# Performance work log

Hardware: AMD Instinct MI355X
Metric: run time of the kernel (lower is better)

The kernel has to match this reference:

```python
import jax, jax.numpy as jnp
import numpy as np

D_MODEL = 768; N_LAYER = 4; D_STATE = 64; D_CONV = 4; EXPAND = 2; HEADDIM = 64
D_INNER = EXPAND * D_MODEL          # 1536
NHEADS = D_INNER // HEADDIM         # 24
CONV_DIM = D_INNER + 2 * D_STATE    # 1664
D_IN_PROJ = 2 * D_INNER + 2 * D_STATE + NHEADS  # 3224
VOCAB = 50257; EPS = 1e-5


def _ln(x, w, b):
    m = x.mean(-1, keepdims=True)
    v = ((x - m) ** 2).mean(-1, keepdims=True)
    return (x - m) * jax.lax.rsqrt(v + EPS) * w + b


def _silu(x):
    return x * jax.nn.sigmoid(x)


def _mamba2(x, W_in, conv_w, conv_b, dt_bias, A_log, Dp, rms_w, W_out):
    # x: [B, L, d_model]
    Bsz, L, _ = x.shape
    zxbcdt = x @ W_in.T                                   # [B,L,D_IN_PROJ]
    z = zxbcdt[..., :D_INNER]
    xBC = zxbcdt[..., D_INNER:D_INNER + CONV_DIM]
    dt = zxbcdt[..., D_INNER + CONV_DIM:]                 # [B,L,H]
    # causal depthwise conv over time
    xc = jnp.transpose(xBC, (0, 2, 1))                    # [B,C,L]
    xc = jax.lax.conv_general_dilated(
        xc, conv_w[:, None, :], (1,), [(D_CONV - 1, 0)],
        dimension_numbers=('NCH', 'OIH', 'NCH'), feature_group_count=CONV_DIM)
    xBC = _silu(jnp.transpose(xc, (0, 2, 1)) + conv_b)
    xh = xBC[..., :D_INNER].reshape(Bsz, L, NHEADS, HEADDIM)
    Bc = xBC[..., D_INNER:D_INNER + D_STATE]              # [B,L,N]
    Cc = xBC[..., D_INNER + D_STATE:]                     # [B,L,N]
    dt = jax.nn.softplus(dt + dt_bias)                    # [B,L,H]
    dA = jnp.exp(dt * (-jnp.exp(A_log)))                  # [B,L,H]

    def step(h, inp):
        dA_t, dt_t, x_t, B_t, C_t = inp
        h = dA_t[:, :, None, None] * h + (dt_t[:, :, None] * x_t)[..., None] * B_t[:, None, None, :]
        return h, jnp.einsum('bhpn,bn->bhp', h, C_t)

    tm = lambda a: jnp.moveaxis(a, 1, 0)  # time-major
    h0 = jnp.zeros((Bsz, NHEADS, HEADDIM, D_STATE), x.dtype)
    _, y = jax.lax.scan(step, h0, (tm(dA), tm(dt), tm(xh), tm(Bc), tm(Cc)))
    y = jnp.moveaxis(y, 0, 1) + Dp[:, None] * xh          # [B,L,H,P]
    y = y.reshape(Bsz, L, D_INNER) * _silu(z)             # gate
    y = y * jax.lax.rsqrt((y * y).mean(-1, keepdims=True) + EPS) * rms_w
    return y @ W_out.T


def setup_inputs() -> dict:
    key = jax.random.key(0)
    ks = jax.random.split(key, 16)
    B, L = 1, 1024
    idx = jax.random.randint(ks[0], (B, L), 0, VOCAB)
    targets = jax.random.randint(ks[1], (B, L), 0, VOCAB)
    s = 0.02
    emb = jax.random.normal(ks[2], (VOCAB, D_MODEL), jnp.float32) * s
    ln_w = jnp.ones((N_LAYER, D_MODEL)); ln_b = jnp.zeros((N_LAYER, D_MODEL))
    W_in = jax.random.normal(ks[3], (N_LAYER, D_IN_PROJ, D_MODEL), jnp.float32) * s
    conv_w = jax.random.normal(ks[4], (N_LAYER, CONV_DIM, D_CONV), jnp.float32) * 0.1
    conv_b = jnp.zeros((N_LAYER, CONV_DIM))
    dt_bias = jnp.log(jnp.expm1(jax.random.uniform(ks[5], (N_LAYER, NHEADS), minval=0.001, maxval=0.1)))
    A_log = jnp.log(jax.random.uniform(ks[6], (N_LAYER, NHEADS), minval=1.0, maxval=16.0))
    Dp = jnp.ones((N_LAYER, NHEADS))
    rms_w = jnp.ones((N_LAYER, D_INNER))
    W_out = jax.random.normal(ks[7], (N_LAYER, D_MODEL, D_INNER), jnp.float32) * s
    lnf_w = jnp.ones((D_MODEL,)); lnf_b = jnp.zeros((D_MODEL,))
    return {"idx": idx, "targets": targets, "emb": emb, "ln_w": ln_w, "ln_b": ln_b,
            "W_in": W_in, "conv_w": conv_w, "conv_b": conv_b, "dt_bias": dt_bias,
            "A_log": A_log, "Dp": Dp, "rms_w": rms_w, "W_out": W_out,
            "lnf_w": lnf_w, "lnf_b": lnf_b}


def reference(idx, targets, emb, ln_w, ln_b, W_in, conv_w, conv_b, dt_bias,
              A_log, Dp, rms_w, W_out, lnf_w, lnf_b):
    x = emb[idx]                                          # [B,L,D]
    for i in range(N_LAYER):
        x = x + _mamba2(_ln(x, ln_w[i], ln_b[i]), W_in[i], conv_w[i], conv_b[i],
                        dt_bias[i], A_log[i], Dp[i], rms_w[i], W_out[i])
    x = _ln(x, lnf_w, lnf_b)
    logits = x @ emb.T                                    # tied head
    logp = jax.nn.log_softmax(logits, axis=-1)
    loss = -jnp.take_along_axis(logp, targets[..., None], axis=-1).mean()
    return logits, loss
```

## Files before the change

kernel.cpp:

```cpp
#include <hip/hip_runtime.h>
#include <hip/hip_bf16.h>
#include <math.h>

#define SL     1024
#define DMODEL 768
#define NLAYER 4
#define NSTATE 64
#define HEADDIM 64
#define DINNER 1536
#define NHEADS 24
#define CONVDIM 1664
#define DINPROJ 3224
#define VOCABN 50257

typedef __attribute__((ext_vector_type(8))) short short8;
typedef __attribute__((ext_vector_type(4))) short short4v;
typedef __attribute__((ext_vector_type(4))) float f32x4;

__device__ __forceinline__ short f2bf(float f) {
    unsigned int u = __builtin_bit_cast(unsigned int, f);
    u += 0x7fffu + ((u >> 16) & 1u);
    return (short)(u >> 16);
}

#define AS1 __attribute__((address_space(1)))
#define AS3 __attribute__((address_space(3)))
__device__ __forceinline__ void gl2lds16(const void* g, void* l) {
    __builtin_amdgcn_global_load_lds((const AS1 unsigned int*)g,
                                     (AS3 unsigned int*)(unsigned int)(uintptr_t)l,
                                     16, 0, 0);
}

template <int CTRL>
__device__ __forceinline__ float dppadd(float x) {
    int v = __builtin_amdgcn_update_dpp(0, __builtin_bit_cast(int, x), CTRL, 0xf, 0xf, true);
    return x + __builtin_bit_cast(float, v);
}

__global__ void cvt_k(const float* __restrict__ s, short* __restrict__ d, int n) {
    int i = (blockIdx.x * 256 + threadIdx.x) * 4;
    if (i >= n) return;
    float4 v = *(const float4*)(s + i);
    short4v o;
    o.x = f2bf(v.x); o.y = f2bf(v.y); o.z = f2bf(v.z); o.w = f2bf(v.w);
    *(short4v*)(d + i) = o;
}

__global__ void embed_k(const int* __restrict__ idx, const float* __restrict__ emb,
                        float* __restrict__ x) {
    int d = blockIdx.x * 256 + threadIdx.x;
    int t = blockIdx.y;
    x[t * DMODEL + d] = emb[(size_t)idx[t] * DMODEL + d];
}

__global__ void ln_k(const float* __restrict__ x, const float* __restrict__ w,
                     const float* __restrict__ b, short* __restrict__ out) {
    int row = blockIdx.x, t = threadIdx.x;
    const float* xr = x + row * DMODEL;
    float v0 = xr[t], v1 = xr[t + 256], v2 = xr[t + 512];
    float s = v0 + v1 + v2;
    float q = v0 * v0 + v1 * v1 + v2 * v2;
    __shared__ float sa[4], sb[4];
    for (int off = 32; off; off >>= 1) { s += __shfl_down(s, off); q += __shfl_down(q, off); }
    if (!(t & 63)) { sa[t >> 6] = s; sb[t >> 6] = q; }
    __syncthreads();
    s = sa[0] + sa[1] + sa[2] + sa[3];
    q = sb[0] + sb[1] + sb[2] + sb[3];
    float mean = s * (1.f / DMODEL);
    float var  = q * (1.f / DMODEL) - mean * mean;
    float rs = rsqrtf(var + 1e-5f);
    out[row * DMODEL + t      ] = f2bf((v0 - mean) * rs * w[t      ] + b[t      ]);
    out[row * DMODEL + t + 256] = f2bf((v1 - mean) * rs * w[t + 256] + b[t + 256]);
    out[row * DMODEL + t + 512] = f2bf((v2 - mean) * rs * w[t + 512] + b[t + 512]);
}

__global__ __launch_bounds__(512) void gemm_bb_k(const short* __restrict__ A,
                                                 const short* __restrict__ B,
                                                 float* __restrict__ C,
                                                 int N, int K, int addflag) {
    __shared__ __align__(16) short As[2][16384];
    __shared__ __align__(16) short Bs[2][16384];
    const int t = threadIdx.x;
    const int lane = t & 63, wv = t >> 6;

    const int nwg = gridDim.x;
    int bid = blockIdx.x;
    int qq = nwg >> 3, rr = nwg & 7;
    int xcd = bid & 7, ii = bid >> 3;
    int v = (xcd < rr ? xcd * (qq + 1) : rr * (qq + 1) + (xcd - rr) * qq) + ii;
    const int m0 = (v & 3) * 256;
    const int n0 = (v >> 2) * 256;

    const int wm = (wv >> 2) * 128, wn = (wv & 3) * 64;
    const int q4 = lane >> 4, l16 = lane & 15;

    f32x4 zero4 = {0.f, 0.f, 0.f, 0.f};
    f32x4 acc[8][4];
#pragma unroll
    for (int i = 0; i < 8; i++)
#pragma unroll
        for (int j = 0; j < 4; j++) acc[i][j] = zero4;

    auto stage = [&](int buf, int k0) {
#pragma unroll
        for (int i = 0; i < 4; i++) {
            int g = i * 512 + t;
            int q = g >> 8, r = g & 255;
            gl2lds16(A + (size_t)(m0 + r) * K + k0 + q * 8, &As[buf][g * 8]);
        }
#pragma unroll
        for (int i = 0; i < 4; i++) {
            int g = i * 512 + t;
            int q = g >> 8, r = g & 255;
            int gr = n0 + r; if (gr > N - 1) gr = N - 1;
            gl2lds16(B + (size_t)gr * K + k0 + q * 8, &Bs[buf][g * 8]);
        }
    };

    const int NT = K >> 6;
    stage(0, 0);
    for (int tt = 0; tt < NT; tt++) {
        const int cur = tt & 1;
        if (tt + 1 < NT) {
            stage(cur ^ 1, (tt + 1) << 6);
            asm volatile("s_waitcnt vmcnt(8)" ::: "memory");
        } else {
            asm volatile("s_waitcnt vmcnt(0)" ::: "memory");
        }
        __builtin_amdgcn_s_barrier();

#pragma unroll
        for (int kk = 0; kk < 2; kk++) {
            short8 af[8], bf[4];
#pragma unroll
            for (int nt = 0; nt < 4; nt++)
                bf[nt] = *(const short8*)(&Bs[cur][(kk * 4 + q4) * 2048 + (wn + nt * 16 + l16) * 8]);
#pragma unroll
            for (int mt = 0; mt < 8; mt++)
                af[mt] = *(const short8*)(&As[cur][(kk * 4 + q4) * 2048 + (wm + mt * 16 + l16) * 8]);
#pragma unroll
            for (int mt = 0; mt < 8; mt++)
#pragma unroll
                for (int nt = 0; nt < 4; nt++)
                    acc[mt][nt] = __builtin_amdgcn_mfma_f32_16x16x32_bf16(af[mt], bf[nt], acc[mt][nt], 0, 0, 0);
        }
        asm volatile("s_waitcnt lgkmcnt(0)" ::: "memory");
        __builtin_amdgcn_s_barrier();
    }

#pragma unroll
    for (int mt = 0; mt < 8; mt++) {
        int row = m0 + wm + mt * 16 + (lane >> 4) * 4;
#pragma unroll
        for (int nt = 0; nt < 4; nt++) {
            int col = n0 + wn + nt * 16 + l16;
            if (col < N) {
#pragma unroll
                for (int r = 0; r < 4; r++) {
                    size_t o = (size_t)(row + r) * N + col;
                    float val = acc[mt][nt][r];
                    if (addflag) C[o] += val; else C[o] = val;
                }
            }
        }
    }
}

__global__ __launch_bounds__(256) void gemm64_k(const short* __restrict__ A,
                                                const short* __restrict__ B,
                                                float* __restrict__ C,
                                                int N, int K, int addflag) {
    __shared__ __align__(16) short As[2][4096];
    __shared__ __align__(16) short Bs[2][4096];
    const int t = threadIdx.x;
    const int lane = t & 63, wv = t >> 6;
    const int m0 = blockIdx.x * 64, n0 = blockIdx.y * 64;
    const int wm = (wv >> 1) * 32, wn = (wv & 1) * 32;
    const int q4 = lane >> 4, l16 = lane & 15;

    f32x4 zero4 = {0.f, 0.f, 0.f, 0.f};
    f32x4 acc[2][2];
#pragma unroll
    for (int i = 0; i < 2; i++)
#pragma unroll
        for (int j = 0; j < 2; j++) acc[i][j] = zero4;

    auto stage = [&](int buf, int k0) {
#pragma unroll
        for (int i = 0; i < 2; i++) {
            int g = i * 256 + t;
            int q = g >> 6, r = g & 63;
            gl2lds16(A + (size_t)(m0 + r) * K + k0 + q * 8, &As[buf][g * 8]);
        }
#pragma unroll
        for (int i = 0; i < 2; i++) {
            int g = i * 256 + t;
            int q = g >> 6, r = g & 63;
            int gr = n0 + r; if (gr > N - 1) gr = N - 1;
            gl2lds16(B + (size_t)gr * K + k0 + q * 8, &Bs[buf][g * 8]);
        }
    };

    const int NT = K >> 6;
    stage(0, 0);
    for (int tt = 0; tt < NT; tt++) {
        const int cur = tt & 1;
        if (tt + 1 < NT) {
            stage(cur ^ 1, (tt + 1) << 6);
            asm volatile("s_waitcnt vmcnt(4)" ::: "memory");
        } else {
            asm volatile("s_waitcnt vmcnt(0)" ::: "memory");
        }
        __builtin_amdgcn_s_barrier();

        short8 af[2][2], bf[2][2];
#pragma unroll
        for (int kk = 0; kk < 2; kk++) {
#pragma unroll
            for (int mt = 0; mt < 2; mt++)
                af[kk][mt] = *(const short8*)(&As[cur][(kk * 4 + q4) * 512 + (wm + mt * 16 + l16) * 8]);
#pragma unroll
            for (int nt = 0; nt < 2; nt++)
                bf[kk][nt] = *(const short8*)(&Bs[cur][(kk * 4 + q4) * 512 + (wn + nt * 16 + l16) * 8]);
        }
        asm volatile("s_waitcnt lgkmcnt(0)" ::: "memory");
        __builtin_amdgcn_s_barrier();

#pragma unroll
        for (int kk = 0; kk < 2; kk++)
#pragma unroll
            for (int mt = 0; mt < 2; mt++)
#pragma unroll
                for (int nt = 0; nt < 2; nt++)
                    acc[mt][nt] = __builtin_amdgcn_mfma_f32_16x16x32_bf16(af[kk][mt], bf[kk][nt], acc[mt][nt], 0, 0, 0);
    }

#pragma unroll
    for (int mt = 0; mt < 2; mt++) {
        int row = m0 + wm + mt * 16 + (lane >> 4) * 4;
#pragma unroll
        for (int nt = 0; nt < 2; nt++) {
            int col = n0 + wn + nt * 16 + l16;
            if (col < N) {
#pragma unroll
                for (int r = 0; r < 4; r++) {
                    size_t o = (size_t)(row + r) * N + col;
                    float val = acc[mt][nt][r];
                    if (addflag) C[o] += val; else C[o] = val;
                }
            }
        }
    }
}

#define LDSK 56
__global__ __launch_bounds__(256) void gemm_bt_k(const short* __restrict__ A,
                                                 const float* __restrict__ B,
                                                 float* __restrict__ C,
                                                 int N, int K, int addflag) {
    __shared__ __align__(16) short As[128 * LDSK];
    __shared__ __align__(16) short Bs[128 * LDSK];
    const int t = threadIdx.x;
    const int lane = t & 63, wv = t >> 6;
    const int m0 = blockIdx.x * 128, n0 = blockIdx.y * 128;
    const int wm = (wv >> 1) * 64, wn = (wv & 1) * 64;
    f32x4 zero4 = {0.f, 0.f, 0.f, 0.f};
    f32x4 acc[4][4];
#pragma unroll
    for (int i = 0; i < 4; i++)
#pragma unroll
        for (int j = 0; j < 4; j++) acc[i][j] = zero4;
    for (int k0 = 0; k0 < K; k0 += 32) {
        uint4  av[2];
        float4 bv[4];
#pragma unroll
        for (int i = 0; i < 2; i++) {
            int c = i * 256 + t, row = c >> 2, kc = c & 3;
            av[i] = *(const uint4*)(A + (size_t)(m0 + row) * K + k0 + kc * 8);
        }
#pragma unroll
        for (int i = 0; i < 4; i++) {
            int c = i * 256 + t, row = c >> 3, kc = c & 7;
            int gr = n0 + row; if (gr > N - 1) gr = N - 1;
            bv[i] = *(const float4*)(B + (size_t)gr * K + k0 + kc * 4);
        }
        __syncthreads();
#pragma unroll
        for (int i = 0; i < 2; i++) {
            int c = i * 256 + t, row = c >> 2, kc = c & 3;
            *(uint4*)(As + row * LDSK + kc * 8) = av[i];
        }
#pragma unroll
        for (int i = 0; i < 4; i++) {
            int c = i * 256 + t, row = c >> 3, kc = c & 7;
            short4v sv;
            sv.x = f2bf(bv[i].x); sv.y = f2bf(bv[i].y);
            sv.z = f2bf(bv[i].z); sv.w = f2bf(bv[i].w);
            *(short4v*)(Bs + row * LDSK + kc * 4) = sv;
        }
        __syncthreads();
        short8 af[4], bf[4];
#pragma unroll
        for (int mt = 0; mt < 4; mt++)
            af[mt] = *(const short8*)(As + (wm + mt * 16 + (lane & 15)) * LDSK + (lane >> 4) * 8);
#pragma unroll
        for (int nt = 0; nt < 4; nt++)
            bf[nt] = *(const short8*)(Bs + (wn + nt * 16 + (lane & 15)) * LDSK + (lane >> 4) * 8);
#pragma unroll
        for (int mt = 0; mt < 4; mt++)
#pragma unroll
            for (int nt = 0; nt < 4; nt++)
                acc[mt][nt] = __builtin_amdgcn_mfma_f32_16x16x32_bf16(af[mt], bf[nt], acc[mt][nt], 0, 0, 0);
    }
#pragma unroll
    for (int mt = 0; mt < 4; mt++) {
        int row = m0 + wm + mt * 16 + (lane >> 4) * 4;
#pragma unroll
        for (int nt = 0; nt < 4; nt++) {
            int col = n0 + wn + nt * 16 + (lane & 15);
            if (col < N) {
#pragma unroll
                for (int r = 0; r < 4; r++) {
                    size_t o = (size_t)(row + r) * N + col;
                    float val = acc[mt][nt][r];
                    if (addflag) C[o] += val; else C[o] = val;
                }
            }
        }
    }
}

__global__ void conv_k(const float* __restrict__ zx, const float* __restrict__ cw,
                       const float* __restrict__ cb, float* __restrict__ xbc) {
    int c = blockIdx.x * 256 + threadIdx.x;
    int t = blockIdx.y;
    if (c >= CONVDIM) return;
    float acc = cb[c];
#pragma unroll
    for (int j = 0; j < 4; j++) {
        int ts = t - 3 + j;
        if (ts >= 0) acc += cw[c * 4 + j] * zx[(size_t)ts * DINPROJ + DINNER + c];
    }
    xbc[(size_t)t * CONVDIM + c] = acc / (1.f + __expf(-acc));
}

__global__ void dt_k(const float* __restrict__ zx, const float* __restrict__ dt_bias,
                     const float* __restrict__ A_log, float* __restrict__ dts,
                     float* __restrict__ dAv) {
    int i = blockIdx.x * 256 + threadIdx.x;
    int tt = i / NHEADS, h = i % NHEADS;
    float d = zx[(size_t)tt * DINPROJ + 3200 + h] + dt_bias[h];
    float sp = (d > 20.f) ? d : log1pf(__expf(d));
    dts[i] = sp;
    dAv[i] = __expf(-__expf(A_log[h]) * sp);
}

__global__ __launch_bounds__(128) void scan_k(const float* __restrict__ xbc,
                                              const float* __restrict__ dts,
                                              const float* __restrict__ dAv,
                                              float* __restrict__ yraw) {
    __shared__ __align__(16) float BCs[64][128];
    __shared__ __align__(16) float xs[64][8];
    __shared__ float dash[64];
    int h = blockIdx.x >> 3;
    int pbase = (blockIdx.x & 7) * 8;
    int t = threadIdx.x, lane = t & 63, wv = t >> 6;
    int pl = wv * 4 + (lane >> 4);
    int n4 = lane & 15;
    float s0 = 0.f, s1 = 0.f, s2 = 0.f, s3 = 0.f;

    for (int tc = 0; tc < 16; tc++) {
        __syncthreads();
#pragma unroll 4
        for (int it = 0; it < 16; it++) {
            int idx = it * 128 + t;
            int trow = idx >> 5, c4 = idx & 31;
            *(float4*)&BCs[trow][c4 * 4] =
                *(const float4*)(xbc + (size_t)(tc * 64 + trow) * CONVDIM + DINNER + c4 * 4);
        }
        {
            int trow = t >> 1, hf = t & 1;
            float dtv = dts[(tc * 64 + trow) * NHEADS + h];
            float4 xv = *(const float4*)(xbc + (size_t)(tc * 64 + trow) * CONVDIM
                                         + h * HEADDIM + pbase + hf * 4);
            xv.x *= dtv; xv.y *= dtv; xv.z *= dtv; xv.w *= dtv;
            *(float4*)&xs[trow][hf * 4] = xv;
        }
        if (t < 64) dash[t] = dAv[(tc * 64 + t) * NHEADS + h];
        __syncthreads();

#pragma unroll 4
        for (int tt = 0; tt < 64; tt++) {
            float4 B4 = *(const float4*)&BCs[tt][n4 * 4];
            float4 C4 = *(const float4*)&BCs[tt][64 + n4 * 4];
            float dtx = xs[tt][pl];
            float da = dash[tt];
            s0 = fmaf(da, s0, dtx * B4.x);
            s1 = fmaf(da, s1, dtx * B4.y);
            s2 = fmaf(da, s2, dtx * B4.z);
            s3 = fmaf(da, s3, dtx * B4.w);
            float part = s0 * C4.x;
            part = fmaf(s1, C4.y, part);
            part = fmaf(s2, C4.z, part);
            part = fmaf(s3, C4.w, part);
            part = dppadd<0xB1>(part);
            part = dppadd<0x4E>(part);
            part = dppadd<0x114>(part);
            part = dppadd<0x118>(part);
            if (n4 == 0)
                yraw[(size_t)(tc * 64 + tt) * DINNER + h * HEADDIM + pbase + pl] = part;
        }
    }
}

__global__ void rms_k(const float* __restrict__ yraw, const float* __restrict__ zx,
                      const float* __restrict__ xbc, const float* __restrict__ Dp,
                      const float* __restrict__ rw, short* __restrict__ yn) {
    int row = blockIdx.x, t = threadIdx.x;
    float v[6];
    float q = 0.f;
#pragma unroll
    for (int j = 0; j < 6; j++) {
        int i = t + j * 256;
        float z  = zx[(size_t)row * DINPROJ + i];
        float xh = xbc[(size_t)row * CONVDIM + i];
        float y  = yraw[(size_t)row * DINNER + i] + Dp[i >> 6] * xh;
        float val = y * (z / (1.f + __expf(-z)));
        v[j] = val;
        q += val * val;
    }
    __shared__ float sb[4];
    for (int off = 32; off; off >>= 1) q += __shfl_down(q, off);
    if (!(t & 63)) sb[t >> 6] = q;
    __syncthreads();
    q = sb[0] + sb[1] + sb[2] + sb[3];
    float rs = rsqrtf(q * (1.f / DINNER) + 1e-5f);
#pragma unroll
    for (int j = 0; j < 6; j++) {
        int i = t + j * 256;
        yn[(size_t)row * DINNER + i] = f2bf(v[j] * rs * rw[i]);
    }
}

__global__ void loss_row_k(const float* __restrict__ logits, const int* __restrict__ tg,
                           float* __restrict__ lossp) {
    int r = blockIdx.x, t = threadIdx.x;
    const float* lr = logits + (size_t)r * VOCABN;
    float m = -3.0e38f, s = 0.f;
    for (int j = t; j < VOCABN; j += 256) {
        float v = lr[j];
        if (v > m) { s = s * __expf(m - v) + 1.f; m = v; }
        else s += __expf(v - m);
    }
    for (int off = 32; off; off >>= 1) {
        float mo = __shfl_down(m, off), so = __shfl_down(s, off);
        float nm = fmaxf(m, mo);
        s = s * __expf(m - nm) + so * __expf(mo - nm);
        m = nm;
    }
    __shared__ float sm[4], ss[4];
    if (!(t & 63)) { sm[t >> 6] = m; ss[t >> 6] = s; }
    __syncthreads();
    if (t == 0) {
        m = sm[0]; s = ss[0];
        for (int w = 1; w < 4; w++) {
            float nm = fmaxf(m, sm[w]);
            s = s * __expf(m - nm) + ss[w] * __expf(sm[w] - nm);
            m = nm;
        }
        lossp[r] = (m + logf(s)) - lr[tg[r]];
    }
}

__global__ void loss_fin_k(const float* __restrict__ lossp, float* __restrict__ out) {
    int t = threadIdx.x;
    float s = lossp[t] + lossp[t + 256] + lossp[t + 512] + lossp[t + 768];
    for (int off = 32; off; off >>= 1) s += __shfl_down(s, off);
    __shared__ float sb[4];
    if (!(t & 63)) sb[t >> 6] = s;
    __syncthreads();
    if (t == 0) out[(size_t)SL * VOCABN] = (sb[0] + sb[1] + sb[2] + sb[3]) * (1.f / SL);
}

extern "C" void kernel_launch(void* const* d_in, const int* in_sizes, int n_in,
                              void* d_out, int out_size, void* d_ws, size_t ws_size,
                              hipStream_t stream) {
    const int*   idx     = (const int*)d_in[0];
    const int*   targets = (const int*)d_in[1];
    const float* emb     = (const float*)d_in[2];
    const float* ln_w    = (const float*)d_in[3];
    const float* ln_b    = (const float*)d_in[4];
    const float* W_in    = (const float*)d_in[5];
    const float* conv_w  = (const float*)d_in[6];
    const float* conv_b  = (const float*)d_in[7];
    const float* dt_bias = (const float*)d_in[8];
    const float* A_log   = (const float*)d_in[9];
    const float* Dp      = (const float*)d_in[10];
    const float* rms_w   = (const float*)d_in[11];
    const float* W_out   = (const float*)d_in[12];
    const float* lnf_w   = (const float*)d_in[13];
    const float* lnf_b   = (const float*)d_in[14];

    char* ws = (char*)d_ws;
    float* x     = (float*)(ws + 0);
    short* xn    = (short*)(ws + 3145728);
    float* zx    = (float*)(ws + 4718592);
    float* xbc   = (float*)(ws + 17924096);
    float* dts   = (float*)(ws + 24739840);
    float* dAv   = (float*)(ws + 24838144);
    float* yraw  = (float*)(ws + 24936448);
    short* yn    = (short*)(ws + 31227904);
    float* lossp = (float*)(ws + 34373632);
    short* wInb  = (short*)(ws + 34377728);
    short* wOutb = (short*)(ws + 54183936);
    short* embb  = (short*)(ws + 63621120);
    float* logits = (float*)d_out;

    const bool big = ws_size >= 140815872ull;

    if (big) {
        int nWin  = NLAYER * DINPROJ * DMODEL;
        int nWout = NLAYER * DMODEL * DINNER;
        int nEmb  = VOCABN * DMODEL;
        cvt_k<<<(nWin / 4 + 255) / 256, 256, 0, stream>>>(W_in, wInb, nWin);
        cvt_k<<<(nWout / 4 + 255) / 256, 256, 0, stream>>>(W_out, wOutb, nWout);
        cvt_k<<<(nEmb / 4 + 255) / 256, 256, 0, stream>>>(emb, embb, nEmb);
    }

    embed_k<<<dim3(3, SL), 256, 0, stream>>>(idx, emb, x);
    for (int l = 0; l < NLAYER; l++) {
        ln_k<<<SL, 256, 0, stream>>>(x, ln_w + l * DMODEL, ln_b + l * DMODEL, xn);
        if (big)
            gemm64_k<<<dim3(16, 51), 256, 0, stream>>>(xn, wInb + (size_t)l * DINPROJ * DMODEL,
                                                       zx, DINPROJ, DMODEL, 0);
        else
            gemm_bt_k<<<dim3(8, 26), 256, 0, stream>>>(xn, W_in + (size_t)l * DINPROJ * DMODEL,
                                                       zx, DINPROJ, DMODEL, 0);
        conv_k<<<dim3(7, SL), 256, 0, stream>>>(zx, conv_w + l * CONVDIM * 4,
                                                conv_b + l * CONVDIM, xbc);
        dt_k<<<96, 256, 0, stream>>>(zx, dt_bias + l * NHEADS, A_log + l * NHEADS, dts, dAv);
        scan_k<<<192, 128, 0, stream>>>(xbc, dts, dAv, yraw);
        rms_k<<<SL, 256, 0, stream>>>(yraw, zx, xbc, Dp + l * NHEADS, rms_w + l * DINNER, yn);
        if (big)
            gemm64_k<<<dim3(16, 12), 256, 0, stream>>>(yn, wOutb + (size_t)l * DMODEL * DINNER,
                                                       x, DMODEL, DINNER, 1);
        else
            gemm_bt_k<<<dim3(8, 6), 256, 0, stream>>>(yn, W_out + (size_t)l * DMODEL * DINNER,
                                                      x, DMODEL, DINNER, 1);
    }
    ln_k<<<SL, 256, 0, stream>>>(x, lnf_w, lnf_b, xn);
    if (big)
        gemm_bb_k<<<4 * 197, 512, 0, stream>>>(xn, embb, logits, VOCABN, DMODEL, 0);
    else
        gemm_bt_k<<<dim3(8, 393), 256, 0, stream>>>(xn, emb, logits, VOCABN, DMODEL, 0);
    loss_row_k<<<SL, 256, 0, stream>>>(logits, targets, lossp);
    loss_fin_k<<<1, 256, 0, stream>>>(lossp, logits);
}
```

Baseline: 1.198 ms.

## Fuse log-softmax partial reductions into LM-head GEMM epilogue with triple buffering

The LM-head GEMM now computes per-row partial max and sum-exp for its 256-column tile in the epilogue and writes them to a workspace buffer. A small kernel then combines the 197 partials per row. This replaces the separate pass that reread the full 1024x50257 logits matrix. The GEMM mainloop also changes from double buffering with K=64 steps to triple buffering with K=32 steps, which halves LDS per stage and adds one more prefetch stage in flight.

```diff
diff --git a/kernel.cpp b/kernel.cpp
--- a/kernel.cpp
+++ b/kernel.cpp
@@ -77,9 +77,10 @@
 __global__ __launch_bounds__(512) void gemm_bb_k(const short* __restrict__ A,
                                                  const short* __restrict__ B,
                                                  float* __restrict__ C,
+                                                 float2* __restrict__ P,
                                                  int N, int K, int addflag) {
-    __shared__ __align__(16) short As[2][16384];
-    __shared__ __align__(16) short Bs[2][16384];
+    __shared__ __align__(16) short As[3][8192];
+    __shared__ __align__(16) short Bs[3][8192];
     const int t = threadIdx.x;
     const int lane = t & 63, wv = t >> 6;
 
@@ -103,13 +104,13 @@
 
     auto stage = [&](int buf, int k0) {
 #pragma unroll
-        for (int i = 0; i < 4; i++) {
+        for (int i = 0; i < 2; i++) {
             int g = i * 512 + t;
             int q = g >> 8, r = g & 255;
             gl2lds16(A + (size_t)(m0 + r) * K + k0 + q * 8, &As[buf][g * 8]);
         }
 #pragma unroll
-        for (int i = 0; i < 4; i++) {
+        for (int i = 0; i < 2; i++) {
             int g = i * 512 + t;
             int q = g >> 8, r = g & 255;
             int gr = n0 + r; if (gr > N - 1) gr = N - 1;
@@ -117,40 +118,43 @@
         }
     };
 
-    const int NT = K >> 6;
+    const int NT = K >> 5;
     stage(0, 0);
+    stage(1, 32);
+    int cur = 0;
     for (int tt = 0; tt < NT; tt++) {
-        const int cur = tt & 1;
-        if (tt + 1 < NT) {
-            stage(cur ^ 1, (tt + 1) << 6);
+        if (tt + 2 < NT) {
+            int b2 = cur + 2; if (b2 >= 3) b2 -= 3;
+            stage(b2, (tt + 2) << 5);
             asm volatile("s_waitcnt vmcnt(8)" ::: "memory");
+        } else if (tt + 1 < NT) {
+            asm volatile("s_waitcnt vmcnt(4)" ::: "memory");
         } else {
             asm volatile("s_waitcnt vmcnt(0)" ::: "memory");
         }
         __builtin_amdgcn_s_barrier();
 
-#pragma unroll
-        for (int kk = 0; kk < 2; kk++) {
-            short8 af[8], bf[4];
+        short8 af[8], bf[4];
+#pragma unroll
+        for (int nt = 0; nt < 4; nt++)
+            bf[nt] = *(const short8*)(&Bs[cur][q4 * 2048 + (wn + nt * 16 + l16) * 8]);
+#pragma unroll
+        for (int mt = 0; mt < 8; mt++)
+            af[mt] = *(const short8*)(&As[cur][q4 * 2048 + (wm + mt * 16 + l16) * 8]);
+#pragma unroll
+        for (int mt = 0; mt < 8; mt++)
 #pragma unroll
             for (int nt = 0; nt < 4; nt++)
-                bf[nt] = *(const short8*)(&Bs[cur][(kk * 4 + q4) * 2048 + (wn + nt * 16 + l16) * 8]);
-#pragma unroll
-            for (int mt = 0; mt < 8; mt++)
-                af[mt] = *(const short8*)(&As[cur][(kk * 4 + q4) * 2048 + (wm + mt * 16 + l16) * 8]);
-#pragma unroll
-            for (int mt = 0; mt < 8; mt++)
-#pragma unroll
-                for (int nt = 0; nt < 4; nt++)
-                    acc[mt][nt] = __builtin_amdgcn_mfma_f32_16x16x32_bf16(af[mt], bf[nt], acc[mt][nt], 0, 0, 0);
-        }
+                acc[mt][nt] = __builtin_amdgcn_mfma_f32_16x16x32_bf16(af[mt], bf[nt], acc[mt][nt], 0, 0, 0);
+
         asm volatile("s_waitcnt lgkmcnt(0)" ::: "memory");
         __builtin_amdgcn_s_barrier();
+        cur++; if (cur == 3) cur = 0;
     }
 
 #pragma unroll
     for (int mt = 0; mt < 8; mt++) {
-        int row = m0 + wm + mt * 16 + (lane >> 4) * 4;
+        int row = m0 + wm + mt * 16 + q4 * 4;
 #pragma unroll
         for (int nt = 0; nt < 4; nt++) {
             int col = n0 + wn + nt * 16 + l16;
@@ -163,6 +167,46 @@
                 }
             }
         }
+    }
+
+    float2* lds_ms = (float2*)&As[0][0];
+    const int nw = wv & 3;
+#pragma unroll
+    for (int mt = 0; mt < 8; mt++) {
+#pragma unroll
+        for (int r = 0; r < 4; r++) {
+            float m = -3.0e38f, s = 0.f;
+#pragma unroll
+            for (int nt = 0; nt < 4; nt++) {
+                int col = n0 + wn + nt * 16 + l16;
+                if (col < N) {
+                    float vv = acc[mt][nt][r];
+                    if (vv > m) { s = s * __expf(m - vv) + 1.f; m = vv; }
+                    else s += __expf(vv - m);
+                }
+            }
+#pragma unroll
+            for (int off = 1; off < 16; off <<= 1) {
+                float mo = __shfl_xor(m, off), so = __shfl_xor(s, off);
+                float nm = fmaxf(m, mo);
+                s = s * __expf(m - nm) + so * __expf(mo - nm);
+                m = nm;
+            }
+            if (l16 == 0)
+                lds_ms[(wm + mt * 16 + q4 * 4 + r) * 4 + nw] = make_float2(m, s);
+        }
+    }
+    __syncthreads();
+    if (t < 256) {
+        float m = -3.0e38f, s = 0.f;
+#pragma unroll
+        for (int w = 0; w < 4; w++) {
+            float2 p = lds_ms[t * 4 + w];
+            float nm = fmaxf(m, p.x);
+            s = s * __expf(m - nm) + p.y * __expf(p.x - nm);
+            m = nm;
+        }
+        P[(size_t)(v >> 2) * 1024 + (m0 + t)] = make_float2(m, s);
     }
 }
 
@@ -472,6 +516,19 @@
     }
 }
 
+__global__ void loss_fin2_k(const float2* __restrict__ P, const float* __restrict__ logits,
+                            const int* __restrict__ tg, float* __restrict__ lossp) {
+    int r = blockIdx.x * 256 + threadIdx.x;
+    float m = -3.0e38f, s = 0.f;
+    for (int p = 0; p < 197; p++) {
+        float2 q = P[(size_t)p * 1024 + r];
+        float nm = fmaxf(m, q.x);
+        s = s * __expf(m - nm) + q.y * __expf(q.x - nm);
+        m = nm;
+    }
+    lossp[r] = (m + logf(s)) - logits[(size_t)r * VOCABN + tg[r]];
+}
+
 __global__ void loss_fin_k(const float* __restrict__ lossp, float* __restrict__ out) {
     int t = threadIdx.x;
     float s = lossp[t] + lossp[t + 256] + lossp[t + 512] + lossp[t + 768];
@@ -514,6 +571,7 @@
     short* wInb  = (short*)(ws + 34377728);
     short* wOutb = (short*)(ws + 54183936);
     short* embb  = (short*)(ws + 63621120);
+    float2* pms  = (float2*)(ws + 4718592);
     float* logits = (float*)d_out;
 
     const bool big = ws_size >= 140815872ull;
@@ -549,10 +607,12 @@
                                                       x, DMODEL, DINNER, 1);
     }
     ln_k<<<SL, 256, 0, stream>>>(x, lnf_w, lnf_b, xn);
-    if (big)
-        gemm_bb_k<<<4 * 197, 512, 0, stream>>>(xn, embb, logits, VOCABN, DMODEL, 0);
-    else
+    if (big) {
+        gemm_bb_k<<<4 * 197, 512, 0, stream>>>(xn, embb, logits, pms, VOCABN, DMODEL, 0);
+        loss_fin2_k<<<4, 256, 0, stream>>>(pms, logits, targets, lossp);
+    } else {
         gemm_bt_k<<<dim3(8, 393), 256, 0, stream>>>(xn, emb, logits, VOCABN, DMODEL, 0);
-    loss_row_k<<<SL, 256, 0, stream>>>(logits, targets, lossp);
+        loss_row_k<<<SL, 256, 0, stream>>>(logits, targets, lossp);
+    }
     loss_fin_k<<<1, 256, 0, stream>>>(lossp, logits);
 }
```

Result: faster. 1.174 ms (-2.0%).
